# Kernel tuning notes

Measured on AMD Instinct MI355X. Metric: run time of the kernel, lower is better.

The kernel has to match this reference:

```python
import jax, jax.numpy as jnp
import numpy as np

N = 50000
E = 200000
IN_C = 32
HID = 32
OUT_C = 16
EDGE_DIM = 8
EPS = 1e-5


def setup_inputs() -> dict:
    key = jax.random.key(0)
    ks = jax.random.split(key, 12)
    x = jax.random.normal(ks[0], (N, IN_C), dtype=jnp.float32)
    edge_index = jax.random.randint(ks[1], (2, E), 0, N, dtype=jnp.int32)
    edge_attr = jax.random.normal(ks[2], (E, EDGE_DIM), dtype=jnp.float32)
    s = 0.05
    # edge MLP: Linear(edge_dim, in*hidden) + ReLU
    nn_w = jax.random.normal(ks[3], (EDGE_DIM, IN_C * HID), dtype=jnp.float32) * s
    nn_b = jax.random.normal(ks[4], (IN_C * HID,), dtype=jnp.float32) * s
    # NNConv root weight and bias
    root = jax.random.normal(ks[5], (IN_C, HID), dtype=jnp.float32) * s
    bias = jax.random.normal(ks[6], (HID,), dtype=jnp.float32) * s
    # LayerNorm params
    norm_w = jnp.ones((HID,), dtype=jnp.float32)
    norm_b = jnp.zeros((HID,), dtype=jnp.float32)
    # final Linear(hidden, out)
    lin_w = jax.random.normal(ks[7], (HID, OUT_C), dtype=jnp.float32) * s
    lin_b = jax.random.normal(ks[8], (OUT_C,), dtype=jnp.float32) * s
    return {"x": x, "edge_index": edge_index, "edge_attr": edge_attr,
            "nn_w": nn_w, "nn_b": nn_b, "root": root, "bias": bias,
            "norm_w": norm_w, "norm_b": norm_b, "lin_w": lin_w, "lin_b": lin_b}


def reference(x, edge_index, edge_attr, nn_w, nn_b, root, bias,
              norm_w, norm_b, lin_w, lin_b):
    src, dst = edge_index[0], edge_index[1]  # messages flow src -> dst
    # per-edge weight matrices via edge MLP: [E, IN_C, HID]
    W = jax.nn.relu(edge_attr @ nn_w + nn_b).reshape(E, IN_C, HID)
    # gather source node features, per-edge matvec: [E, HID]
    msg = jnp.einsum('ei,eio->eo', x[src], W)
    # scatter-add aggregation to target nodes: [N, HID]
    agg = jax.ops.segment_sum(msg, dst, num_segments=N)
    h = agg + x @ root + bias
    # LayerNorm over feature dim
    mu = jnp.mean(h, axis=-1, keepdims=True)
    var = jnp.mean(jnp.square(h - mu), axis=-1, keepdims=True)
    h = (h - mu) * jax.lax.rsqrt(var + EPS) * norm_w + norm_b
    h = jax.nn.relu(h)
    return h @ lin_w + lin_b
```

## Files before the change

kernel.cpp:

```cpp
#include <hip/hip_runtime.h>
#include <hip/hip_bf16.h>

#define N_NODES 50000
#define N_EDGES 200000
#define NTILES  (N_EDGES / 32)
#define EBLK    768
#define TWAVES  (EBLK * 4)

typedef float  v2f    __attribute__((ext_vector_type(2)));
typedef float  f32x16 __attribute__((ext_vector_type(16)));
typedef short  s16x8  __attribute__((ext_vector_type(8)));

static __device__ inline v2f sp2(float s) { v2f r; r.x = s; r.y = s; return r; }

static __device__ inline v2f fma2(v2f a, v2f b, v2f c) {
#if __has_builtin(__builtin_elementwise_fma)
    return __builtin_elementwise_fma(a, b, c);
#else
    v2f r; r.x = fmaf(a.x, b.x, c.x); r.y = fmaf(a.y, b.y, c.y); return r;
#endif
}

static __device__ inline v2f max2(v2f a, v2f b) {
#if __has_builtin(__builtin_elementwise_max)
    return __builtin_elementwise_max(a, b);
#else
    v2f r; r.x = fmaxf(a.x, b.x); r.y = fmaxf(a.y, b.y); return r;
#endif
}

static __device__ inline unsigned short bf_rne(float f) {
    unsigned int u = __float_as_uint(f);
    u += 0x7fffu + ((u >> 16) & 1u);
    return (unsigned short)(u >> 16);
}

__global__ __launch_bounds__(256, 3) void edge_kernel(
    const float* __restrict__ x, const int* __restrict__ ei,
    const float* __restrict__ ea, const float* __restrict__ nn_w,
    const float* __restrict__ nn_b, float* __restrict__ agg)
{
    __shared__ unsigned short wT[1024 * 16];
    __shared__ float tl4[4][32 * 33];

    for (int c = threadIdx.x; c < 1024; c += 256) {
        unsigned short row[16];
#pragma unroll
        for (int k = 0; k < 8; ++k) row[k] = bf_rne(nn_w[k * 1024 + c]);
#pragma unroll
        for (int k = 0; k < 7; ++k) row[8 + k] = row[k];
        row[15] = bf_rne(nn_b[c]);
        unsigned int w[8];
#pragma unroll
        for (int q = 0; q < 8; ++q)
            w[q] = (unsigned int)row[2 * q] | ((unsigned int)row[2 * q + 1] << 16);
        uint4* p = (uint4*)(wT + c * 16);
        uint4 lo_; lo_.x = w[0]; lo_.y = w[1]; lo_.z = w[2]; lo_.w = w[3];
        uint4 hi_; hi_.x = w[4]; hi_.y = w[5]; hi_.z = w[6]; hi_.w = w[7];
        p[0] = lo_; p[1] = hi_;
    }
    __syncthreads();

    const int lane = threadIdx.x & 63;
    const int eo   = lane & 31;
    const int hsel = lane >> 5;
    float* tl = tl4[threadIdx.x >> 6];

    int t = (int)((blockIdx.x * 256u + threadIdx.x) >> 6);
    if (t >= NTILES) return;

    int    sc  = ei[t * 32 + eo];
    int    dc  = ei[N_EDGES + t * 32 + eo];
    float4 ea0 = ((const float4*)(ea + (size_t)(t * 32 + eo) * 8))[0];
    float4 ea1 = ((const float4*)(ea + (size_t)(t * 32 + eo) * 8))[1];

    float4 xq[8];
    {
        const float4* xp = (const float4*)(x + (size_t)sc * 32);
#pragma unroll
        for (int q = 0; q < 8; ++q) xq[q] = xp[q];
    }

    int tn = t + TWAVES;
    int tc = tn < NTILES ? tn : t;
    int    sn  = ei[tc * 32 + eo];
    int    dn  = ei[N_EDGES + tc * 32 + eo];
    float4 na0 = ((const float4*)(ea + (size_t)(tc * 32 + eo) * 8))[0];
    float4 na1 = ((const float4*)(ea + (size_t)(tc * 32 + eo) * 8))[1];

    const f32x16 zf = {0.f,0.f,0.f,0.f,0.f,0.f,0.f,0.f,
                       0.f,0.f,0.f,0.f,0.f,0.f,0.f,0.f};

    while (true) {
        const float ef[8] = {ea0.x, ea0.y, ea0.z, ea0.w,
                             ea1.x, ea1.y, ea1.z, ea1.w};
        s16x8 bfrag;
#pragma unroll
        for (int j = 0; j < 8; ++j) {
            const float f = ef[j];
            const unsigned short hi = bf_rne(f);
            unsigned short v;
            if (j < 7) {
                const unsigned short lo =
                    bf_rne(f - __uint_as_float(((unsigned int)hi) << 16));
                v = hsel ? lo : hi;
            } else {
                v = hsel ? (unsigned short)0x3F80 : hi;
            }
            bfrag[j] = (short)v;
        }

        const float4* xpn = (const float4*)(x + (size_t)sn * 32);

        v2f m2[8];
#pragma unroll
        for (int p = 0; p < 8; ++p) m2[p] = sp2(0.f);

#pragma unroll
        for (int i = 0; i < 32; ++i) {
            const s16x8 a = *(const s16x8*)(wT + (i * 32 + eo) * 16 + hsel * 8);
            const f32x16 d =
                __builtin_amdgcn_mfma_f32_32x32x16_bf16(a, bfrag, zf, 0, 0, 0);
            const float4 xc = xq[i >> 2];
            const float xv = (i & 3) == 0 ? xc.x : (i & 3) == 1 ? xc.y
                           : (i & 3) == 2 ? xc.z : xc.w;
            const v2f x2 = sp2(xv);
#pragma unroll
            for (int p = 0; p < 8; ++p) {
                v2f dd; dd.x = d[2 * p]; dd.y = d[2 * p + 1];
                m2[p] = fma2(x2, max2(dd, sp2(0.f)), m2[p]);
            }
            if ((i & 3) == 3) xq[i >> 2] = xpn[i >> 2];
        }

#pragma unroll
        for (int p = 0; p < 8; ++p) {
            const int r0 = 2 * p, r1 = 2 * p + 1;
            const int o0 = (r0 & 3) + 8 * (r0 >> 2) + 4 * hsel;
            const int o1 = (r1 & 3) + 8 * (r1 >> 2) + 4 * hsel;
            tl[o0 * 33 + eo] = m2[p].x;
            tl[o1 * 33 + eo] = m2[p].y;
        }

#pragma unroll
        for (int r = 0; r < 16; ++r) {
            const int d0 = __builtin_amdgcn_readlane(dc, 2 * r);
            const int d1 = __builtin_amdgcn_readlane(dc, 2 * r + 1);
            const int dr = hsel ? d1 : d0;
            const float v = tl[eo * 33 + 2 * r + hsel];
            unsafeAtomicAdd(&agg[(size_t)dr * 32 + eo], v);
        }

        if (tn >= NTILES) break;
        t = tn; sc = sn; dc = dn; ea0 = na0; ea1 = na1;
        tn = t + TWAVES; tc = tn < NTILES ? tn : t;
        sn  = ei[tc * 32 + eo];
        dn  = ei[N_EDGES + tc * 32 + eo];
        na0 = ((const float4*)(ea + (size_t)(tc * 32 + eo) * 8))[0];
        na1 = ((const float4*)(ea + (size_t)(tc * 32 + eo) * 8))[1];
    }
}

__global__ __launch_bounds__(256) void finalize_kernel(
    const float* __restrict__ agg, const float* __restrict__ x,
    const float* __restrict__ root, const float* __restrict__ bias,
    const float* __restrict__ norm_w, const float* __restrict__ norm_b,
    const float* __restrict__ lin_w, const float* __restrict__ lin_b,
    float* __restrict__ out)
{
    __shared__ v2f rlds[512];
    __shared__ v2f llds[256];
    __shared__ v2f blds[16], nwl[16], nbl[16], lbl[8];

    const int t = threadIdx.x;
    for (int f = t; f < 1024; f += 256) ((float*)rlds)[f] = root[f];
    for (int f = t; f < 512;  f += 256) ((float*)llds)[f] = lin_w[f];
    if (t < 32) {
        ((float*)blds)[t] = bias[t];
        ((float*)nwl)[t]  = norm_w[t];
        ((float*)nbl)[t]  = norm_b[t];
    }
    if (t < 16) ((float*)lbl)[t] = lin_b[t];
    __syncthreads();

    const int n = blockIdx.x * 256 + t;
    if (n >= N_NODES) return;

    float4 xf[8], af[8];
    {
        const float4* xp = (const float4*)(x + (size_t)n * 32);
        const float4* ap = (const float4*)(agg + (size_t)n * 32);
#pragma unroll
        for (int q = 0; q < 8; ++q) { xf[q] = xp[q]; af[q] = ap[q]; }
    }

    v2f h[16];
#pragma unroll
    for (int oo = 0; oo < 16; ++oo) {
        v2f a; a.x = ((const float*)af)[2 * oo]; a.y = ((const float*)af)[2 * oo + 1];
        h[oo] = a + blds[oo];
    }
#pragma unroll
    for (int i = 0; i < 32; ++i) {
        const float xi = ((const float*)xf)[i];
#pragma unroll
        for (int oo = 0; oo < 16; ++oo)
            h[oo] = fma2(sp2(xi), rlds[i * 16 + oo], h[oo]);
    }

    v2f sv = h[0];
#pragma unroll
    for (int oo = 1; oo < 16; ++oo) sv += h[oo];
    const float mu = (sv.x + sv.y) * (1.f / 32.f);
    const v2f mu2 = sp2(mu);
    v2f qv = (h[0] - mu2) * (h[0] - mu2);
#pragma unroll
    for (int oo = 1; oo < 16; ++oo) {
        const v2f dd = h[oo] - mu2;
        qv = fma2(dd, dd, qv);
    }
    const float var = (qv.x + qv.y) * (1.f / 32.f);
    const float rs = rsqrtf(var + 1e-5f);

    v2f r[16];
#pragma unroll
    for (int oo = 0; oo < 16; ++oo) {
        const v2f nv = fma2((h[oo] - mu2) * sp2(rs), nwl[oo], nbl[oo]);
        r[oo] = max2(nv, sp2(0.f));
    }

    v2f a2[8];
#pragma unroll
    for (int jj = 0; jj < 8; ++jj) a2[jj] = lbl[jj];
#pragma unroll
    for (int o = 0; o < 32; ++o) {
        const float rv = (o & 1) ? r[o >> 1].y : r[o >> 1].x;
#pragma unroll
        for (int jj = 0; jj < 8; ++jj)
            a2[jj] = fma2(sp2(rv), llds[o * 8 + jj], a2[jj]);
    }

    float4* op = (float4*)(out + (size_t)n * 16);
#pragma unroll
    for (int q = 0; q < 4; ++q) {
        float4 v;
        v.x = a2[2 * q].x; v.y = a2[2 * q].y;
        v.z = a2[2 * q + 1].x; v.w = a2[2 * q + 1].y;
        op[q] = v;
    }
}

extern "C" void kernel_launch(void* const* d_in, const int* in_sizes, int n_in,
                              void* d_out, int out_size, void* d_ws, size_t ws_size,
                              hipStream_t stream)
{
    const float* x      = (const float*)d_in[0];
    const int*   ei     = (const int*)  d_in[1];
    const float* ea     = (const float*)d_in[2];
    const float* nn_w   = (const float*)d_in[3];
    const float* nn_b   = (const float*)d_in[4];
    const float* root   = (const float*)d_in[5];
    const float* bias   = (const float*)d_in[6];
    const float* norm_w = (const float*)d_in[7];
    const float* norm_b = (const float*)d_in[8];
    const float* lin_w  = (const float*)d_in[9];
    const float* lin_b  = (const float*)d_in[10];
    float* out = (float*)d_out;

    float* agg = (float*)d_ws;

    hipMemsetAsync(agg, 0, (size_t)N_NODES * 32 * sizeof(float), stream);
    edge_kernel<<<EBLK, 256, 0, stream>>>(x, ei, ea, nn_w, nn_b, agg);
    finalize_kernel<<<(N_NODES + 255) / 256, 256, 0, stream>>>(
        agg, x, root, bias, norm_w, norm_b, lin_w, lin_b, out);
}
```

Baseline: 142.1 us.

## Software-pipeline MFMA, use 512-thread blocks and bf16 swizzled transpose tile

Blocks grow to 8 waves of 512 threads, so each CU keeps fewer copies of the shared weight table for the same wave count. The inner loop now issues the next MFMA before applying ReLU and FMA to the previous result, overlapping MFMA latency with VALU work. The per-wave transpose buffer stores messages as bf16 with an XOR swizzle instead of padded fp32, halving LDS use. The cost is lower precision on messages before the atomic add.

```diff
diff --git a/kernel.cpp b/kernel.cpp
--- a/kernel.cpp
+++ b/kernel.cpp
@@ -4,8 +4,9 @@
 #define N_NODES 50000
 #define N_EDGES 200000
 #define NTILES  (N_EDGES / 32)
-#define EBLK    768
-#define TWAVES  (EBLK * 4)
+#define EBLK    512
+#define WPB     8
+#define TWAVES  (EBLK * WPB)
 
 typedef float  v2f    __attribute__((ext_vector_type(2)));
 typedef float  f32x16 __attribute__((ext_vector_type(16)));
@@ -35,15 +36,15 @@
     return (unsigned short)(u >> 16);
 }
 
-__global__ __launch_bounds__(256, 3) void edge_kernel(
+__global__ __launch_bounds__(512, 3) void edge_kernel(
     const float* __restrict__ x, const int* __restrict__ ei,
     const float* __restrict__ ea, const float* __restrict__ nn_w,
     const float* __restrict__ nn_b, float* __restrict__ agg)
 {
     __shared__ unsigned short wT[1024 * 16];
-    __shared__ float tl4[4][32 * 33];
-
-    for (int c = threadIdx.x; c < 1024; c += 256) {
+    __shared__ unsigned short tl8[WPB][1024];
+
+    for (int c = threadIdx.x; c < 1024; c += 512) {
         unsigned short row[16];
 #pragma unroll
         for (int k = 0; k < 8; ++k) row[k] = bf_rne(nn_w[k * 1024 + c]);
@@ -64,9 +65,10 @@
     const int lane = threadIdx.x & 63;
     const int eo   = lane & 31;
     const int hsel = lane >> 5;
-    float* tl = tl4[threadIdx.x >> 6];
-
-    int t = (int)((blockIdx.x * 256u + threadIdx.x) >> 6);
+    unsigned short* tl = tl8[threadIdx.x >> 6];
+    const unsigned short* wTp = wT + eo * 16 + hsel * 8;
+
+    int t = (int)((blockIdx.x * 512u + threadIdx.x) >> 6);
     if (t >= NTILES) return;
 
     int    sc  = ei[t * 32 + eo];
@@ -116,21 +118,26 @@
 #pragma unroll
         for (int p = 0; p < 8; ++p) m2[p] = sp2(0.f);
 
+        s16x8 a0 = *(const s16x8*)(wTp);
+        f32x16 d0 = __builtin_amdgcn_mfma_f32_32x32x16_bf16(a0, bfrag, zf, 0, 0, 0);
 #pragma unroll
         for (int i = 0; i < 32; ++i) {
-            const s16x8 a = *(const s16x8*)(wT + (i * 32 + eo) * 16 + hsel * 8);
-            const f32x16 d =
-                __builtin_amdgcn_mfma_f32_32x32x16_bf16(a, bfrag, zf, 0, 0, 0);
+            f32x16 d1 = d0;
+            if (i < 31) {
+                const s16x8 a1 = *(const s16x8*)(wTp + (i + 1) * 512);
+                d1 = __builtin_amdgcn_mfma_f32_32x32x16_bf16(a1, bfrag, zf, 0, 0, 0);
+            }
             const float4 xc = xq[i >> 2];
             const float xv = (i & 3) == 0 ? xc.x : (i & 3) == 1 ? xc.y
                            : (i & 3) == 2 ? xc.z : xc.w;
             const v2f x2 = sp2(xv);
 #pragma unroll
             for (int p = 0; p < 8; ++p) {
-                v2f dd; dd.x = d[2 * p]; dd.y = d[2 * p + 1];
+                v2f dd; dd.x = d0[2 * p]; dd.y = d0[2 * p + 1];
                 m2[p] = fma2(x2, max2(dd, sp2(0.f)), m2[p]);
             }
             if ((i & 3) == 3) xq[i >> 2] = xpn[i >> 2];
+            d0 = d1;
         }
 
 #pragma unroll
@@ -138,16 +145,18 @@
             const int r0 = 2 * p, r1 = 2 * p + 1;
             const int o0 = (r0 & 3) + 8 * (r0 >> 2) + 4 * hsel;
             const int o1 = (r1 & 3) + 8 * (r1 >> 2) + 4 * hsel;
-            tl[o0 * 33 + eo] = m2[p].x;
-            tl[o1 * 33 + eo] = m2[p].y;
+            tl[o0 * 32 + (eo ^ o0)] = bf_rne(m2[p].x);
+            tl[o1 * 32 + (eo ^ o1)] = bf_rne(m2[p].y);
         }
 
 #pragma unroll
         for (int r = 0; r < 16; ++r) {
-            const int d0 = __builtin_amdgcn_readlane(dc, 2 * r);
-            const int d1 = __builtin_amdgcn_readlane(dc, 2 * r + 1);
-            const int dr = hsel ? d1 : d0;
-            const float v = tl[eo * 33 + 2 * r + hsel];
+            const int d0i = __builtin_amdgcn_readlane(dc, 2 * r);
+            const int d1i = __builtin_amdgcn_readlane(dc, 2 * r + 1);
+            const int dr  = hsel ? d1i : d0i;
+            const int col = 2 * r + hsel;
+            const unsigned short mv = tl[eo * 32 + (col ^ eo)];
+            const float v = __uint_as_float(((unsigned int)mv) << 16);
             unsafeAtomicAdd(&agg[(size_t)dr * 32 + eo], v);
         }
 
@@ -270,7 +279,7 @@
     float* agg = (float*)d_ws;
 
     hipMemsetAsync(agg, 0, (size_t)N_NODES * 32 * sizeof(float), stream);
-    edge_kernel<<<EBLK, 256, 0, stream>>>(x, ei, ea, nn_w, nn_b, agg);
+    edge_kernel<<<EBLK, 512, 0, stream>>>(x, ei, ea, nn_w, nn_b, agg);
     finalize_kernel<<<(N_NODES + 255) / 256, 256, 0, stream>>>(
         agg, x, root, bias, norm_w, norm_b, lin_w, lin_b, out);
 }
```

Measured after the change: 158.4 us. 11.5% more time.
